# Kernel optimization log

Hardware: AMD Instinct MI355X
Metric: run time of the kernel (lower is better)

Reference implementation:

```python
import jax, jax.numpy as jnp
import numpy as np

D_MODEL = 256
N_HEADS = 8
N_LEVELS = 4
NUM_POINTS_LIST = [4, 4, 4, 4]
SUM_POINTS = sum(NUM_POINTS_LIST)
TOTAL_POINTS = N_HEADS * SUM_POINTS
HEAD_DIM = D_MODEL // N_HEADS
OFFSET_SCALE = 0.5
SPATIAL_SHAPES = np.array([[80, 80], [40, 40], [20, 20], [10, 10]], dtype=np.int64)


def setup_inputs() -> dict:
    key = jax.random.key(0)
    ks = jax.random.split(key, 7)
    B, NQ = 16, 300
    seq = int((SPATIAL_SHAPES[:, 0] * SPATIAL_SHAPES[:, 1]).sum())  # 8500
    s = 1.0 / np.sqrt(D_MODEL)
    return {
        'hidden_states': jax.random.normal(ks[0], (B, NQ, D_MODEL), jnp.float32),
        'encoder_hidden_states': jax.random.normal(ks[1], (B, seq, D_MODEL), jnp.float32),
        'reference_points': jax.random.uniform(ks[2], (B, NQ, 1, 4), jnp.float32, 0.05, 0.95),
        'spatial_shapes': SPATIAL_SHAPES,
        'w_off': jax.random.uniform(ks[3], (TOTAL_POINTS * 2, D_MODEL), jnp.float32, -s, s),
        'b_off': jax.random.uniform(ks[4], (TOTAL_POINTS * 2,), jnp.float32, -s, s),
        'w_attn': jax.random.uniform(ks[5], (TOTAL_POINTS, D_MODEL), jnp.float32, -s, s),
        'b_attn': jax.random.uniform(ks[6], (TOTAL_POINTS,), jnp.float32, -s, s),
    }


def _grid_sample_zeros(img_flat, H, W, gx, gy):
    # img_flat: [N, H*W, C]; gx, gy: [N, Q, P] unnormalized pixel coords.
    # Bilinear, padding_mode='zeros', align_corners=False semantics of torch.grid_sample.
    x0 = jnp.floor(gx)
    y0 = jnp.floor(gy)
    wx = (gx - x0)[..., None]
    wy = (gy - y0)[..., None]
    x0i = x0.astype(jnp.int32)
    y0i = y0.astype(jnp.int32)

    def gather(xi, yi):
        valid = (xi >= 0) & (xi < W) & (yi >= 0) & (yi < H)
        idx = jnp.clip(yi, 0, H - 1) * W + jnp.clip(xi, 0, W - 1)
        N = img_flat.shape[0]
        v = jnp.take_along_axis(img_flat, idx.reshape(N, -1)[..., None], axis=1)
        v = v.reshape(idx.shape + (img_flat.shape[-1],))
        return v * valid[..., None]

    v00 = gather(x0i, y0i)
    v01 = gather(x0i + 1, y0i)
    v10 = gather(x0i, y0i + 1)
    v11 = gather(x0i + 1, y0i + 1)
    top = v00 * (1 - wx) + v01 * wx
    bot = v10 * (1 - wx) + v11 * wx
    return top * (1 - wy) + bot * wy  # [N, Q, P, C]


def reference(hidden_states, encoder_hidden_states, reference_points, spatial_shapes, w_off, b_off, w_attn, b_attn):
    B, NQ, _ = hidden_states.shape
    seq = encoder_hidden_states.shape[1]
    shapes = np.asarray(spatial_shapes)

    value = encoder_hidden_states.reshape(B, seq, N_HEADS, HEAD_DIM)

    off = (hidden_states @ w_off.T + b_off).reshape(B, NQ, N_HEADS, SUM_POINTS, 2)
    attn = jax.nn.softmax((hidden_states @ w_attn.T + b_attn).reshape(B, NQ, N_HEADS, SUM_POINTS), axis=-1)

    # reference_points: [B, NQ, 1, 4] (cx, cy, w, h) in [0,1]
    nps = jnp.asarray(np.repeat([1.0 / n for n in NUM_POINTS_LIST], NUM_POINTS_LIST), hidden_states.dtype)[:, None]
    offset = off * nps * reference_points[:, :, None, :, 2:] * OFFSET_SCALE
    sampling_locations = reference_points[:, :, None, :, :2] + offset  # [B,NQ,H,P,2]

    grids = 2.0 * sampling_locations - 1.0
    value_bh = value.transpose(0, 2, 1, 3).reshape(B * N_HEADS, seq, HEAD_DIM)
    grids_bh = grids.transpose(0, 2, 1, 3, 4).reshape(B * N_HEADS, NQ, SUM_POINTS, 2)

    outs = []
    start_s, start_p = 0, 0
    for lvl in range(N_LEVELS):
        Hl, Wl = int(shapes[lvl, 0]), int(shapes[lvl, 1])
        Pl = NUM_POINTS_LIST[lvl]
        img = value_bh[:, start_s:start_s + Hl * Wl]  # [BH, Hl*Wl, hd]
        g = grids_bh[:, :, start_p:start_p + Pl]
        gx = (g[..., 0] + 1.0) * Wl / 2.0 - 0.5
        gy = (g[..., 1] + 1.0) * Hl / 2.0 - 0.5
        outs.append(_grid_sample_zeros(img, Hl, Wl, gx, gy))
        start_s += Hl * Wl
        start_p += Pl

    sampled = jnp.concatenate(outs, axis=2)  # [BH, NQ, SUM_POINTS, hd]
    attn_bh = attn.transpose(0, 2, 1, 3).reshape(B * N_HEADS, NQ, SUM_POINTS, 1)
    out = (sampled * attn_bh).sum(axis=2)  # [BH, NQ, hd]
    out = out.reshape(B, N_HEADS, NQ, HEAD_DIM).transpose(0, 2, 1, 3).reshape(B, NQ, D_MODEL)
    return (out, attn)
```

## Files before the change

kernel.cpp:

```cpp
#include <hip/hip_runtime.h>
#include <hip/hip_bf16.h>

#define BQ_TOTAL 4800
#define D_MODEL 256
#define N_HEADS 8
#define SUM_POINTS 16
#define HEAD_DIM 32
#define SEQ 8500
#define OUT_ELEMS (BQ_TOTAL * D_MODEL)

typedef _Float16 half8 __attribute__((ext_vector_type(8)));
typedef _Float16 half4 __attribute__((ext_vector_type(4)));
typedef float floatx4 __attribute__((ext_vector_type(4)));

#define LDK 264

__global__ __launch_bounds__(256) void gemm_logits_mfma(
    const float* __restrict__ hs,
    const float* __restrict__ w_off, const float* __restrict__ b_off,
    const float* __restrict__ w_attn, const float* __restrict__ b_attn,
    float* __restrict__ off_out, float* __restrict__ attn_out)
{
    __shared__ _Float16 Asld[64 * LDK];
    __shared__ _Float16 Bsld[64 * LDK];

    const int tid = threadIdx.x;
    const int row0 = blockIdx.x * 64;
    const int col0 = blockIdx.y * 64;

    const float* Bsrc; const float* bias;
    if (col0 < 256) { Bsrc = w_off  + (size_t)col0 * 256;        bias = b_off  + col0; }
    else            { Bsrc = w_attn + (size_t)(col0 - 256) * 256; bias = b_attn + (col0 - 256); }

    #pragma unroll
    for (int i = 0; i < 16; i++) {
        const int idx = tid + i * 256;
        const int r = idx >> 6;
        const int kc = (idx & 63) << 2;

        const float4 a = *(const float4*)(hs + (size_t)(row0 + r) * 256 + kc);
        half4 ah; ah[0] = (_Float16)a.x; ah[1] = (_Float16)a.y;
                  ah[2] = (_Float16)a.z; ah[3] = (_Float16)a.w;
        *(half4*)&Asld[r * LDK + kc] = ah;

        const float4 b = *(const float4*)(Bsrc + (size_t)r * 256 + kc);
        half4 bh; bh[0] = (_Float16)b.x; bh[1] = (_Float16)b.y;
                  bh[2] = (_Float16)b.z; bh[3] = (_Float16)b.w;
        *(half4*)&Bsld[r * LDK + kc] = bh;
    }
    __syncthreads();

    const int wv = tid >> 6;
    const int lane = tid & 63;
    const int m = lane & 15;
    const int quad = lane >> 4;

    half8 af[8];
    #pragma unroll
    for (int q8 = 0; q8 < 8; q8++)
        af[q8] = *(const half8*)&Asld[(wv * 16 + m) * LDK + q8 * 32 + quad * 8];

    floatx4 acc[4] = {{0.f,0.f,0.f,0.f},{0.f,0.f,0.f,0.f},{0.f,0.f,0.f,0.f},{0.f,0.f,0.f,0.f}};
    #pragma unroll
    for (int ct = 0; ct < 4; ct++) {
        #pragma unroll
        for (int q8 = 0; q8 < 8; q8++) {
            const half8 bf = *(const half8*)&Bsld[(ct * 16 + m) * LDK + q8 * 32 + quad * 8];
            acc[ct] = __builtin_amdgcn_mfma_f32_16x16x32_f16(af[q8], bf, acc[ct], 0, 0, 0);
        }
    }

    #pragma unroll
    for (int ct = 0; ct < 4; ct++) {
        const int col_l = ct * 16 + m;
        const float bv = bias[col_l];
        #pragma unroll
        for (int rg = 0; rg < 4; rg++) {
            const int row = row0 + wv * 16 + quad * 4 + rg;
            const float v = acc[ct][rg] + bv;
            if (col0 < 256)
                off_out[(size_t)row * 256 + col0 + col_l] = v;
            else
                attn_out[(size_t)row * 128 + (col0 - 256) + col_l] = v;
        }
    }
}

__global__ __launch_bounds__(256) void deform_sample(
    const float* __restrict__ enc,
    const float* __restrict__ refp,
    const float* __restrict__ offlog,
    float* __restrict__ attn,
    float* __restrict__ out)
{
    const int tid = threadIdx.x;
    const int w = tid >> 6;
    const int lane = tid & 63;
    const int item = blockIdx.x * 4 + w;
    const int bq = item >> 3;
    const int h = item & 7;
    const int p = lane >> 2;
    const int sub = lane & 3;

    float* attn_ptr = attn + (size_t)bq * 128 + h * 16;
    const float l = attn_ptr[p];
    float m = l;
    #pragma unroll
    for (int s = 4; s < 64; s <<= 1) m = fmaxf(m, __shfl_xor(m, s));
    const float e = __expf(l - m);
    float ssum = e;
    #pragma unroll
    for (int s = 4; s < 64; s <<= 1) ssum += __shfl_xor(ssum, s);
    const float prob = e / ssum;
    if (sub == 0) attn_ptr[p] = prob;

    const float2 off2 = *(const float2*)(offlog + (size_t)bq * 256 + h * 32 + 2 * p);
    const float* rp = refp + (size_t)bq * 4;
    const float cx = rp[0], cy = rp[1], rw = rp[2], rh = rp[3];

    const int lvl = p >> 2;
    const int Wl = 80 >> lvl;
    int base = 0;
    if (lvl == 1) base = 6400;
    else if (lvl == 2) base = 8000;
    else if (lvl == 3) base = 8400;

    const float Wf = (float)Wl;
    const float gx = (cx + off2.x * 0.125f * rw) * Wf - 0.5f;
    const float gy = (cy + off2.y * 0.125f * rh) * Wf - 0.5f;
    const float x0f = floorf(gx), y0f = floorf(gy);
    const float fx = gx - x0f, fy = gy - y0f;
    const int x0 = (int)x0f, y0 = (int)y0f;

    const int b = bq / 300;
    const float* pbase = enc + ((size_t)b * SEQ + base) * 256 + h * 32 + sub * 4;

    float4 acc0 = {0.f, 0.f, 0.f, 0.f};
    float4 acc1 = {0.f, 0.f, 0.f, 0.f};
    #pragma unroll
    for (int c = 0; c < 4; c++) {
        const int xc = x0 + (c & 1);
        const int yc = y0 + (c >> 1);
        const float wx = (c & 1) ? fx : (1.0f - fx);
        const float wy = (c >> 1) ? fy : (1.0f - fy);
        const bool valid = (xc >= 0) && (xc < Wl) && (yc >= 0) && (yc < Wl);
        const int xi = min(max(xc, 0), Wl - 1);
        const int yi = min(max(yc, 0), Wl - 1);
        const float wgt = valid ? wx * wy : 0.0f;
        const float* vp = pbase + (size_t)(yi * Wl + xi) * 256;
        const float4 va = *(const float4*)(vp);
        const float4 vb = *(const float4*)(vp + 16);
        acc0.x += wgt * va.x; acc0.y += wgt * va.y;
        acc0.z += wgt * va.z; acc0.w += wgt * va.w;
        acc1.x += wgt * vb.x; acc1.y += wgt * vb.y;
        acc1.z += wgt * vb.z; acc1.w += wgt * vb.w;
    }

    float vals[8];
    vals[0] = acc0.x * prob; vals[1] = acc0.y * prob;
    vals[2] = acc0.z * prob; vals[3] = acc0.w * prob;
    vals[4] = acc1.x * prob; vals[5] = acc1.y * prob;
    vals[6] = acc1.z * prob; vals[7] = acc1.w * prob;

    #pragma unroll
    for (int s = 4; s < 64; s <<= 1) {
        #pragma unroll
        for (int j = 0; j < 8; j++) vals[j] += __shfl_xor(vals[j], s);
    }

    if (lane < 8) {
        const int halfs = lane >> 2;
        const int sb = lane & 3;
        float4 v;
        if (halfs == 0) { v.x = vals[0]; v.y = vals[1]; v.z = vals[2]; v.w = vals[3]; }
        else            { v.x = vals[4]; v.y = vals[5]; v.z = vals[6]; v.w = vals[7]; }
        out[(size_t)bq * 256 + h * 32 + halfs * 16 + sb * 4 + 0] = v.x;
        out[(size_t)bq * 256 + h * 32 + halfs * 16 + sb * 4 + 1] = v.y;
        out[(size_t)bq * 256 + h * 32 + halfs * 16 + sb * 4 + 2] = v.z;
        out[(size_t)bq * 256 + h * 32 + halfs * 16 + sb * 4 + 3] = v.w;
    }
}

extern "C" void kernel_launch(void* const* d_in, const int* in_sizes, int n_in,
                              void* d_out, int out_size, void* d_ws, size_t ws_size,
                              hipStream_t stream) {
    const float* hs     = (const float*)d_in[0];
    const float* enc    = (const float*)d_in[1];
    const float* refp   = (const float*)d_in[2];
    const float* w_off  = (const float*)d_in[4];
    const float* b_off  = (const float*)d_in[5];
    const float* w_attn = (const float*)d_in[6];
    const float* b_attn = (const float*)d_in[7];

    float* out  = (float*)d_out;
    float* attn = out + OUT_ELEMS;
    float* offlog = (float*)d_ws;

    dim3 g1(BQ_TOTAL / 64, 384 / 64);
    gemm_logits_mfma<<<g1, 256, 0, stream>>>(hs, w_off, b_off, w_attn, b_attn, offlog, attn);

    deform_sample<<<(BQ_TOTAL * N_HEADS) / 4, 256, 0, stream>>>(enc, refp, offlog, attn, out);
}
```

Before: 216.9 us.

## Remap deform blocks by head and use a halving shuffle reduction

Block indices in the sampling kernel are remapped so that consecutive blocks handle the same head group across different queries. The intent is to change the locality of encoder value reads in L2. The cross-lane reduction is rewritten as a recursive-halving transpose reduce, cutting the shuffle count from 32 to 15 per lane, and the output is written by 32 lanes instead of 8. The attention probability is folded into the bilinear weight, and the reference point is read as a single float4.

Result: slower. 225.9 us (+4.1%).

```diff
diff --git a/kernel.cpp b/kernel.cpp
--- a/kernel.cpp
+++ b/kernel.cpp
@@ -29,7 +29,7 @@
     const int col0 = blockIdx.y * 64;
 
     const float* Bsrc; const float* bias;
-    if (col0 < 256) { Bsrc = w_off  + (size_t)col0 * 256;        bias = b_off  + col0; }
+    if (col0 < 256) { Bsrc = w_off  + (size_t)col0 * 256;         bias = b_off  + col0; }
     else            { Bsrc = w_attn + (size_t)(col0 - 256) * 256; bias = b_attn + (col0 - 256); }
 
     #pragma unroll
@@ -96,7 +96,8 @@
     const int tid = threadIdx.x;
     const int w = tid >> 6;
     const int lane = tid & 63;
-    const int item = blockIdx.x * 4 + w;
+    const int blk = (blockIdx.x & 7) * 1200 + (blockIdx.x >> 3);
+    const int item = blk * 4 + w;
     const int bq = item >> 3;
     const int h = item & 7;
     const int p = lane >> 2;
@@ -104,10 +105,10 @@
 
     float* attn_ptr = attn + (size_t)bq * 128 + h * 16;
     const float l = attn_ptr[p];
-    float m = l;
+    float mx = l;
     #pragma unroll
-    for (int s = 4; s < 64; s <<= 1) m = fmaxf(m, __shfl_xor(m, s));
-    const float e = __expf(l - m);
+    for (int s = 4; s < 64; s <<= 1) mx = fmaxf(mx, __shfl_xor(mx, s));
+    const float e = __expf(l - mx);
     float ssum = e;
     #pragma unroll
     for (int s = 4; s < 64; s <<= 1) ssum += __shfl_xor(ssum, s);
@@ -115,8 +116,7 @@
     if (sub == 0) attn_ptr[p] = prob;
 
     const float2 off2 = *(const float2*)(offlog + (size_t)bq * 256 + h * 32 + 2 * p);
-    const float* rp = refp + (size_t)bq * 4;
-    const float cx = rp[0], cy = rp[1], rw = rp[2], rh = rp[3];
+    const float4 rp = *(const float4*)(refp + (size_t)bq * 4);
 
     const int lvl = p >> 2;
     const int Wl = 80 >> lvl;
@@ -126,8 +126,8 @@
     else if (lvl == 3) base = 8400;
 
     const float Wf = (float)Wl;
-    const float gx = (cx + off2.x * 0.125f * rw) * Wf - 0.5f;
-    const float gy = (cy + off2.y * 0.125f * rh) * Wf - 0.5f;
+    const float gx = (rp.x + off2.x * 0.125f * rp.z) * Wf - 0.5f;
+    const float gy = (rp.y + off2.y * 0.125f * rp.w) * Wf - 0.5f;
     const float x0f = floorf(gx), y0f = floorf(gy);
     const float fx = gx - x0f, fy = gy - y0f;
     const int x0 = (int)x0f, y0 = (int)y0f;
@@ -135,8 +135,7 @@
     const int b = bq / 300;
     const float* pbase = enc + ((size_t)b * SEQ + base) * 256 + h * 32 + sub * 4;
 
-    float4 acc0 = {0.f, 0.f, 0.f, 0.f};
-    float4 acc1 = {0.f, 0.f, 0.f, 0.f};
+    float vals[8] = {0.f,0.f,0.f,0.f,0.f,0.f,0.f,0.f};
     #pragma unroll
     for (int c = 0; c < 4; c++) {
         const int xc = x0 + (c & 1);
@@ -146,38 +145,35 @@
         const bool valid = (xc >= 0) && (xc < Wl) && (yc >= 0) && (yc < Wl);
         const int xi = min(max(xc, 0), Wl - 1);
         const int yi = min(max(yc, 0), Wl - 1);
-        const float wgt = valid ? wx * wy : 0.0f;
+        const float wgt = valid ? wx * wy * prob : 0.0f;
         const float* vp = pbase + (size_t)(yi * Wl + xi) * 256;
         const float4 va = *(const float4*)(vp);
         const float4 vb = *(const float4*)(vp + 16);
-        acc0.x += wgt * va.x; acc0.y += wgt * va.y;
-        acc0.z += wgt * va.z; acc0.w += wgt * va.w;
-        acc1.x += wgt * vb.x; acc1.y += wgt * vb.y;
-        acc1.z += wgt * vb.z; acc1.w += wgt * vb.w;
+        vals[0] += wgt * va.x; vals[1] += wgt * va.y;
+        vals[2] += wgt * va.z; vals[3] += wgt * va.w;
+        vals[4] += wgt * vb.x; vals[5] += wgt * vb.y;
+        vals[6] += wgt * vb.z; vals[7] += wgt * vb.w;
     }
 
-    float vals[8];
-    vals[0] = acc0.x * prob; vals[1] = acc0.y * prob;
-    vals[2] = acc0.z * prob; vals[3] = acc0.w * prob;
-    vals[4] = acc1.x * prob; vals[5] = acc1.y * prob;
-    vals[6] = acc1.z * prob; vals[7] = acc1.w * prob;
+    const int b2 = (lane >> 2) & 1, b3 = (lane >> 3) & 1, b4 = (lane >> 4) & 1;
+    #pragma unroll
+    for (int j = 0; j < 8; j++) vals[j] += __shfl_xor(vals[j], 4);
+    float w4[4];
+    #pragma unroll
+    for (int j = 0; j < 4; j++) w4[j] = b2 ? vals[j + 4] : vals[j];
+    #pragma unroll
+    for (int j = 0; j < 4; j++) w4[j] += __shfl_xor(w4[j], 8);
+    float w2[2];
+    #pragma unroll
+    for (int j = 0; j < 2; j++) w2[j] = b3 ? w4[j + 2] : w4[j];
+    #pragma unroll
+    for (int j = 0; j < 2; j++) w2[j] += __shfl_xor(w2[j], 16);
+    float t = b4 ? w2[1] : w2[0];
+    t += __shfl_xor(t, 32);
 
-    #pragma unroll
-    for (int s = 4; s < 64; s <<= 1) {
-        #pragma unroll
-        for (int j = 0; j < 8; j++) vals[j] += __shfl_xor(vals[j], s);
-    }
-
-    if (lane < 8) {
-        const int halfs = lane >> 2;
-        const int sb = lane & 3;
-        float4 v;
-        if (halfs == 0) { v.x = vals[0]; v.y = vals[1]; v.z = vals[2]; v.w = vals[3]; }
-        else            { v.x = vals[4]; v.y = vals[5]; v.z = vals[6]; v.w = vals[7]; }
-        out[(size_t)bq * 256 + h * 32 + halfs * 16 + sb * 4 + 0] = v.x;
-        out[(size_t)bq * 256 + h * 32 + halfs * 16 + sb * 4 + 1] = v.y;
-        out[(size_t)bq * 256 + h * 32 + halfs * 16 + sb * 4 + 2] = v.z;
-        out[(size_t)bq * 256 + h * 32 + halfs * 16 + sb * 4 + 3] = v.w;
+    if (lane < 32) {
+        const int ch = b2 * 16 + sub * 4 + b3 * 2 + b4;
+        out[(size_t)bq * 256 + h * 32 + ch] = t;
     }
 }
 
```
